# Kernel optimization log

Hardware: AMD Instinct MI355X
Metric: run time of the kernel (lower is better)

Reference implementation:

```python
import jax, jax.numpy as jnp
import numpy as np

EPS = 1e-20
K = 3        # kernel_size
STRIDE = 2
PAD = 1
DIL = 1
B, C, O, H, W = 4, 32, 32, 256, 256
HO = (H + 2 * PAD - DIL * (K - 1) - 1) // STRIDE + 1  # 128
WO = (W + 2 * PAD - DIL * (K - 1) - 1) // STRIDE + 1  # 128


def kernel_channels(x):
    """Unfold-like gather: [B,C,H,W] -> [B,C,K*K,HO,WO] (zero-padded)."""
    xp = jnp.pad(x, ((0, 0), (0, 0), (PAD, PAD), (PAD, PAD)))
    patches = [
        xp[:, :, i * DIL : i * DIL + (HO - 1) * STRIDE + 1 : STRIDE,
              j * DIL : j * DIL + (WO - 1) * STRIDE + 1 : STRIDE]
        for i in range(K) for j in range(K)
    ]
    return jnp.stack(patches, axis=2)


def setup_inputs() -> dict:
    key = jax.random.key(0)
    ks = jax.random.split(key, 11)
    return {
        "d":   jax.random.normal(ks[0], (B, C, H, W), jnp.float32),
        "cd":  jax.random.uniform(ks[1], (B, C, H, W), jnp.float32),
        "s":   jax.random.uniform(ks[2], (B, C, H, W), jnp.float32),
        "cs":  jax.random.uniform(ks[3], (B, C, H, W), jnp.float32),
        "gx":  jax.random.normal(ks[4], (B, C, H, W), jnp.float32),
        "cgx": jax.random.uniform(ks[5], (B, C, H, W), jnp.float32),
        "s_prod_roll": jax.random.uniform(ks[6], (B, C, K * K, HO, WO), jnp.float32),
        # learned parameters (raw; softplus applied in forward via EnforcePos)
        "w_prop":         jax.random.normal(ks[7], (1, C, 1, 1), jnp.float32) * 0.5,
        "spatial_weight": jax.random.normal(ks[8], (C, 1, K * K, 1, 1), jnp.float32) * 0.5,
        "channel_weight": jax.random.normal(ks[9], (O, C, 1, 1), jnp.float32) * 0.5,
        "bias":           jax.random.normal(ks[10], (1, O, 1, 1), jnp.float32) * 0.01,
    }


def reference(d, cd, s, cs, gx, cgx, s_prod_roll,
              w_prop, spatial_weight, channel_weight, bias):
    # EnforcePos: positive reparametrization of the weights
    wp = jax.nn.softplus(w_prop)                          # [1,C,1,1]
    sw = jax.nn.softplus(spatial_weight)[:, 0, :, 0, 0]   # [C,K*K]
    cw = jax.nn.softplus(channel_weight)[:, :, 0, 0]      # [O,C]

    # width-dim shift/pad (exactly matches F.pad(x[...,: -1], (0,1)) etc.)
    pad_r = lambda x: jnp.pad(x[:, :, :, :-1], ((0, 0), (0, 0), (0, 0), (0, 1)))
    pad_l = lambda x: jnp.pad(x[:, :, :, 1:],  ((0, 0), (0, 0), (0, 0), (1, 0)))
    d_left,  cd_left,  s_left  = pad_r(d), pad_r(cd), pad_r(s)
    d_right, cd_right, s_right = pad_l(d), pad_l(cd), pad_l(s)

    cgx_from_ds = s * s_left * s_right * cd_left * cd_right
    height = (cd_left * d_left + cd_right * d_right) / (cd_left + cd_right + EPS)
    gx_from_ds = (d_right - d_left) / 2 / (height + EPS)

    gx = (wp * cgx * gx + cgx_from_ds * gx_from_ds) / (wp * cgx + cgx_from_ds + EPS)
    cgx = (wp * cgx + cgx_from_ds) / (wp + 1.0)

    gx_roll = kernel_channels(gx)        # [B,C,K*K,HO,WO]
    cgx_roll = kernel_channels(cgx)
    cgx_prop = cgx_roll * s_prod_roll

    # spatial stage: grouped conv3d over kernel-channel dim == per-channel 9-tap reduce
    nom = jnp.einsum('bckhw,ck->bchw', cgx_prop * gx_roll, sw)
    den = jnp.einsum('bckhw,ck->bchw', cgx_prop, sw)
    gx_sp = nom / (den + EPS)
    cgx_sp = den / (jnp.sum(sw) + EPS)

    # channel stage: 1x1 conv2d (groups=1)
    nom2 = jnp.einsum('bchw,oc->bohw', cgx_sp * gx_sp, cw)
    den2 = jnp.einsum('bchw,oc->bohw', cgx_sp, cw)
    gx_out = nom2 / (den2 + EPS) + bias
    cgx_out = den2 / (jnp.sum(cw) + EPS)

    # devalue_pooled_confidence=True
    return gx_out * STRIDE, cgx_out / (STRIDE * STRIDE)
```

## Files before the change

### kernel.cpp

```cpp
#include <hip/hip_runtime.h>
#include <math.h>

#define EPSF 1e-20f
#define Bv 4
#define Cv 32
#define Ov 32
#define Hv 256
#define Wv 256
#define HOv 128
#define WOv 128
#define NPIX (HOv * WOv)
#define HALF_OUT (Bv * Ov * NPIX)

typedef float f4v __attribute__((ext_vector_type(4)));
typedef float f2v __attribute__((ext_vector_type(2)));

__device__ __forceinline__ float softplus_f(float x) {
    return fmaxf(x, 0.0f) + log1pf(__expf(-fabsf(x)));
}
__device__ __forceinline__ float frcp(float x) {
    return __builtin_amdgcn_rcpf(x);
}

__device__ __forceinline__ float4 gload4(const float* p) {
    float4 r;
    asm volatile("global_load_dwordx4 %0, %1, off" : "=v"(r) : "v"(p));
    return r;
}
__device__ __forceinline__ float2 gload2(const float* p) {
    float2 r;
    asm volatile("global_load_dwordx2 %0, %1, off" : "=v"(r) : "v"(p));
    return r;
}
__device__ __forceinline__ void vm_drain() {
    asm volatile("s_waitcnt vmcnt(0)" ::: "memory");
    __builtin_amdgcn_sched_barrier(0);
}

#define WS_BUF_OFF 2048
#define WS_NEEDED (WS_BUF_OFF * 4 + (size_t)Bv * Cv * NPIX * 8)

__global__ void prep_kernel(const float* __restrict__ wp_raw,
                            const float* __restrict__ sw_raw,
                            const float* __restrict__ cw_raw,
                            float* __restrict__ ws) {
    __shared__ float red_sw[256];
    __shared__ float red_cw[256];
    const int t = threadIdx.x;
    float acc_sw = 0.f, acc_cw = 0.f;
    if (t < 32) ws[t] = softplus_f(wp_raw[t]);
    for (int i = t; i < 288; i += 256) {
        float v = softplus_f(sw_raw[i]);
        ws[32 + i] = v;
        acc_sw += v;
    }
    for (int i = t; i < 1024; i += 256) {
        float v = softplus_f(cw_raw[i]);
        ws[320 + i] = v;
        acc_cw += v;
    }
    red_sw[t] = acc_sw;
    red_cw[t] = acc_cw;
    __syncthreads();
    for (int st = 128; st > 0; st >>= 1) {
        if (t < st) { red_sw[t] += red_sw[t + st]; red_cw[t] += red_cw[t + st]; }
        __syncthreads();
    }
    if (t == 0) {
        ws[1344] = 1.0f / (red_sw[0] + EPSF);
        ws[1345] = 1.0f / (red_cw[0] + EPSF);
    }
}

__global__ __launch_bounds__(256, 2)
void k1_spatial(const float* __restrict__ d,  const float* __restrict__ cd,
                const float* __restrict__ s,  const float* __restrict__ gx,
                const float* __restrict__ cgx, const float* __restrict__ sprod,
                const float* __restrict__ ws, float2* __restrict__ buf) {
    __shared__ float lds[16128];
    float* inL = lds;
    float* gaL = lds + 11520;
    float* caL = lds + 13824;

    const int t  = threadIdx.x;
    const int l  = t & 63;
    const int q  = t >> 6;
    const int z  = blockIdx.x >> 5;
    const int rt = blockIdx.x & 31;
    const int c  = z & 31;

    const float wpc = ws[c];
    const float inv_wp1 = frcp(wpc + 1.0f);
    const float inv_sumsw = ws[1344];
    const float* sw_c = ws + 32 + c * 9;

    const int ho0     = rt * 4;
    const int h_top   = 2 * ho0 - 1;
    const bool top    = (rt == 0);
    const int h_start = top ? 0 : h_top;
    const int nf4     = top ? 512 : 576;
    const int dof     = top ? 256 : 0;
    const int gbase   = z * (Hv * Wv) + h_start * Wv;

    float4 st[5][3];
#pragma unroll
    for (int a = 0; a < 5; ++a) {
        const float* gp = (a == 0) ? d : (a == 1) ? cd : (a == 2) ? s
                        : (a == 3) ? gx : cgx;
#pragma unroll
        for (int k = 0; k < 3; ++k) {
            const int o = t + k * 256;
            if (o < nf4) st[a][k] = gload4(gp + gbase + 4 * o);
        }
    }
    const int ho  = ho0 + q;
    const int sp0 = (z * 9 * HOv + ho) * WOv + 2 * l;
    f2v sp[9];
#pragma unroll
    for (int k = 0; k < 9; ++k)
        sp[k] = __builtin_nontemporal_load(
                    (const f2v*)(sprod + sp0 + k * NPIX));

    vm_drain();

#pragma unroll
    for (int a = 0; a < 5; ++a) {
#pragma unroll
        for (int k = 0; k < 3; ++k) {
            const int o = t + k * 256;
            if (o < nf4)
                *(float4*)(inL + a * 2304 + dof + 4 * o) = st[a][k];
        }
    }
    __syncthreads();

#pragma unroll
    for (int j = 0; j < 9; ++j) {
        const int o = j * 256 + t;
        const float dV  = inL[0 * 2304 + o];
        const float cdV = inL[1 * 2304 + o];
        const float sV  = inL[2 * 2304 + o];
        const float gV  = inL[3 * 2304 + o];
        const float cV  = inL[4 * 2304 + o];
        const bool mL = (t != Wv - 1);
        const bool mR = (t != 0);
        const float dL  = mL ? dV  : 0.f;
        const float cdL = mL ? cdV : 0.f;
        const float sL  = mL ? sV  : 0.f;
        const float dR  = mR ? dV  : 0.f;
        const float cdR = mR ? cdV : 0.f;
        const float sR  = mR ? sV  : 0.f;
        const float cgx_ds = sV * sL * sR * cdL * cdR;
        const float height = (cdL * dL + cdR * dR) * frcp(cdL + cdR + EPSF);
        const float gx_ds  = (dR - dL) * 0.5f * frcp(height + EPSF);
        const float a_ = wpc * cV;
        const float g_ = (a_ * gV + cgx_ds * gx_ds) * frcp(a_ + cgx_ds + EPSF);
        const float c_ = (a_ + cgx_ds) * inv_wp1;
        const bool vrow = (j > 0) || !top;
        gaL[o] = vrow ? g_ : 0.f;
        caL[o] = vrow ? c_ : 0.f;
    }
    __syncthreads();

    float n0 = 0.f, d0 = 0.f, n1 = 0.f, d1 = 0.f;
#pragma unroll
    for (int ki = 0; ki < 3; ++ki) {
        const int ro = (2 * q + ki) * 256;
        const float4 g4 = *(const float4*)(gaL + ro + 4 * l);
        const float4 c4 = *(const float4*)(caL + ro + 4 * l);
        const int eo = ro + (l ? 4 * l - 1 : 0);
        float geL = gaL[eo];
        float ceL = caL[eo];
        geL = l ? geL : 0.f;
        ceL = l ? ceL : 0.f;
        const float sw0 = sw_c[3 * ki + 0];
        const float sw1 = sw_c[3 * ki + 1];
        const float sw2 = sw_c[3 * ki + 2];
        float cp;
        cp = ceL  * sp[3 * ki + 0].x * sw0; d0 += cp; n0 = fmaf(cp, geL,  n0);
        cp = c4.x * sp[3 * ki + 1].x * sw1; d0 += cp; n0 = fmaf(cp, g4.x, n0);
        cp = c4.y * sp[3 * ki + 2].x * sw2; d0 += cp; n0 = fmaf(cp, g4.y, n0);
        cp = c4.y * sp[3 * ki + 0].y * sw0; d1 += cp; n1 = fmaf(cp, g4.y, n1);
        cp = c4.z * sp[3 * ki + 1].y * sw1; d1 += cp; n1 = fmaf(cp, g4.z, n1);
        cp = c4.w * sp[3 * ki + 2].y * sw2; d1 += cp; n1 = fmaf(cp, g4.w, n1);
    }
    const float gx0 = n0 * frcp(d0 + EPSF);
    const float cg0 = d0 * inv_sumsw;
    const float gx1 = n1 * frcp(d1 + EPSF);
    const float cg1 = d1 * inv_sumsw;
    float4 ov = {cg0 * gx0, cg0, cg1 * gx1, cg1};
    *(float4*)(buf + (size_t)z * NPIX + ho * WOv + 2 * l) = ov;
}

__global__ __launch_bounds__(256, 2)
void k2_channel(const float2* __restrict__ buf, const float* __restrict__ ws,
                const float* __restrict__ bias, float* __restrict__ out) {
    const int pg  = blockIdx.x * 256 + threadIdx.x;
    const int b   = pg >> 14;
    const int pp  = pg & (NPIX - 1);
    const int grp = blockIdx.y;
    const float* cw_t = ws + 320;
    const float inv_sumcw = ws[1345];

    const int cbase = b * Cv * NPIX + pp;

    float2 v[Cv];
#pragma unroll
    for (int cc = 0; cc < Cv; ++cc)
        v[cc] = gload2((const float*)(buf + cbase + cc * NPIX));

    vm_drain();

    float nom2[16], den2[16];
#pragma unroll
    for (int i = 0; i < 16; ++i) { nom2[i] = 0.f; den2[i] = 0.f; }

#pragma unroll
    for (int cc = 0; cc < Cv; ++cc) {
#pragma unroll
        for (int oi = 0; oi < 16; ++oi) {
            const float w_ = cw_t[(grp * 16 + oi) * Cv + cc];
            nom2[oi] = fmaf(v[cc].x, w_, nom2[oi]);
            den2[oi] = fmaf(v[cc].y, w_, den2[oi]);
        }
    }
#pragma unroll
    for (int oi = 0; oi < 16; ++oi) {
        const int o = grp * 16 + oi;
        const int p = (b * Ov + o) * NPIX + pp;
        const float dn = den2[oi];
        const float g  = nom2[oi] * frcp(dn + EPSF) + bias[o];
        __builtin_nontemporal_store(g * 2.0f, out + p);
        __builtin_nontemporal_store(dn * inv_sumcw * 0.25f, out + HALF_OUT + p);
    }
}

#define TH 4
#define TW 32
#define IH 9
#define IW 65
#define IWP 66
#define NTILE (IH * IW)

__global__ __launch_bounds__(128)
void main_kernel(const float* __restrict__ d,  const float* __restrict__ cd,
                 const float* __restrict__ s,  const float* __restrict__ gx,
                 const float* __restrict__ cgx, const float* __restrict__ sprod,
                 const float* __restrict__ bias, const float* __restrict__ ws,
                 float* __restrict__ out) {
    __shared__ float lgx[IH][IWP];
    __shared__ float lcgx[IH][IWP];
    const int t    = threadIdx.x;
    const int wo_l = t & 31;
    const int ho_l = t >> 5;
    const int wo0  = blockIdx.x * TW;
    const int ho0  = blockIdx.y * TH;
    const int b    = blockIdx.z;
    const int ho   = ho0 + ho_l;
    const int wo   = wo0 + wo_l;
    const float* sw_t = ws + 32;
    const float* cw_t = ws + 320;
    const float inv_sumsw = ws[1344];
    const float inv_sumcw = ws[1345];
    float nom2[Ov], den2[Ov];
#pragma unroll
    for (int o = 0; o < Ov; ++o) { nom2[o] = 0.f; den2[o] = 0.f; }
    const int h_base = 2 * ho0 - 1;
    const int w_base = 2 * wo0 - 1;
    for (int c = 0; c < Cv; ++c) {
        const float wpc = ws[c];
        const float inv_wp1 = frcp(wpc + 1.0f);
        const int ibase = (b * Cv + c) * (Hv * Wv);
        for (int idx = t; idx < NTILE; idx += 128) {
            const int r  = idx / IW;
            const int cc = idx - r * IW;
            const int h  = h_base + r;
            const int w  = w_base + cc;
            float gxn = 0.f, cgxn = 0.f;
            if ((unsigned)h < (unsigned)Hv && (unsigned)w < (unsigned)Wv) {
                const int p = ibase + h * Wv + w;
                const float dv = d[p], cdv = cd[p], sv = s[p];
                const float gxv = gx[p], cgxv = cgx[p];
                const bool mLb = (w != Wv - 1);
                const bool mRb = (w != 0);
                const float dL = mLb ? dv : 0.f, cdL = mLb ? cdv : 0.f, sL = mLb ? sv : 0.f;
                const float dR = mRb ? dv : 0.f, cdR = mRb ? cdv : 0.f, sR = mRb ? sv : 0.f;
                const float cgx_ds = sv * sL * sR * cdL * cdR;
                const float height = (cdL * dL + cdR * dR) * frcp(cdL + cdR + EPSF);
                const float gx_ds  = (dR - dL) * 0.5f * frcp(height + EPSF);
                const float a = wpc * cgxv;
                gxn  = (a * gxv + cgx_ds * gx_ds) * frcp(a + cgx_ds + EPSF);
                cgxn = (a + cgx_ds) * inv_wp1;
            }
            lgx[r][cc]  = gxn;
            lcgx[r][cc] = cgxn;
        }
        __syncthreads();
        const int spb = ((b * Cv + c) * 9 * HOv + ho) * WOv + wo;
        float nom = 0.f, den = 0.f;
#pragma unroll
        for (int k = 0; k < 9; ++k) {
            const int ki = k / 3;
            const int kj = k - ki * 3;
            const float gxr  = lgx[2 * ho_l + ki][2 * wo_l + kj];
            const float cgxr = lcgx[2 * ho_l + ki][2 * wo_l + kj];
            const float spv  = sprod[spb + k * NPIX];
            const float cp   = cgxr * spv * sw_t[c * 9 + k];
            den += cp;
            nom = fmaf(cp, gxr, nom);
        }
        const float gx_sp  = nom * frcp(den + EPSF);
        const float cgx_sp = den * inv_sumsw;
        const float t1 = cgx_sp * gx_sp;
#pragma unroll
        for (int o = 0; o < Ov; ++o) {
            const float w_ = cw_t[o * Cv + c];
            nom2[o] = fmaf(t1, w_, nom2[o]);
            den2[o] = fmaf(cgx_sp, w_, den2[o]);
        }
        __syncthreads();
    }
#pragma unroll
    for (int o = 0; o < Ov; ++o) {
        const int p = ((b * Ov + o) * HOv + ho) * WOv + wo;
        const float dn = den2[o];
        const float g  = nom2[o] * frcp(dn + EPSF) + bias[o];
        out[p]            = g * 2.0f;
        out[HALF_OUT + p] = dn * inv_sumcw * 0.25f;
    }
}

extern "C" void kernel_launch(void* const* d_in, const int* in_sizes, int n_in,
                              void* d_out, int out_size, void* d_ws, size_t ws_size,
                              hipStream_t stream) {
    const float* d_ptr    = (const float*)d_in[0];
    const float* cd_ptr   = (const float*)d_in[1];
    const float* s_ptr    = (const float*)d_in[2];
    const float* gx_ptr   = (const float*)d_in[4];
    const float* cgx_ptr  = (const float*)d_in[5];
    const float* sp_ptr   = (const float*)d_in[6];
    const float* wp_ptr   = (const float*)d_in[7];
    const float* sw_ptr   = (const float*)d_in[8];
    const float* cw_ptr   = (const float*)d_in[9];
    const float* bias_ptr = (const float*)d_in[10];
    float* out = (float*)d_out;
    float* ws  = (float*)d_ws;

    prep_kernel<<<1, 256, 0, stream>>>(wp_ptr, sw_ptr, cw_ptr, ws);

    if (ws_size >= WS_NEEDED) {
        float2* buf = (float2*)(ws + WS_BUF_OFF);
        k1_spatial<<<4096, 256, 0, stream>>>(d_ptr, cd_ptr, s_ptr, gx_ptr, cgx_ptr,
                                             sp_ptr, ws, buf);
        dim3 g2((Bv * NPIX) / 256, 2, 1);
        k2_channel<<<g2, 256, 0, stream>>>(buf, ws, bias_ptr, out);
    } else {
        dim3 grid(WOv / TW, HOv / TH, Bv);
        main_kernel<<<grid, 128, 0, stream>>>(d_ptr, cd_ptr, s_ptr, gx_ptr, cgx_ptr,
                                              sp_ptr, bias_ptr, ws, out);
    }
}
```

Baseline: 265.2 us.

## Halve spatial tile height to two output rows, one pixel per thread

```diff
diff --git a/kernel.cpp b/kernel.cpp
--- a/kernel.cpp
+++ b/kernel.cpp
@@ -72,76 +72,70 @@
     }
 }
 
-__global__ __launch_bounds__(256, 2)
+__global__ __launch_bounds__(256, 4)
 void k1_spatial(const float* __restrict__ d,  const float* __restrict__ cd,
                 const float* __restrict__ s,  const float* __restrict__ gx,
                 const float* __restrict__ cgx, const float* __restrict__ sprod,
                 const float* __restrict__ ws, float2* __restrict__ buf) {
-    __shared__ float lds[16128];
+    __shared__ float lds[8960];
     float* inL = lds;
-    float* gaL = lds + 11520;
-    float* caL = lds + 13824;
-
-    const int t  = threadIdx.x;
-    const int l  = t & 63;
-    const int q  = t >> 6;
-    const int z  = blockIdx.x >> 5;
-    const int rt = blockIdx.x & 31;
-    const int c  = z & 31;
+    float* gaL = lds + 6400;
+    float* caL = lds + 7680;
+
+    const int t   = threadIdx.x;
+    const int z   = blockIdx.x >> 6;
+    const int rtp = blockIdx.x & 63;
+    const int c   = z & 31;
 
     const float wpc = ws[c];
     const float inv_wp1 = frcp(wpc + 1.0f);
     const float inv_sumsw = ws[1344];
     const float* sw_c = ws + 32 + c * 9;
 
-    const int ho0     = rt * 4;
-    const int h_top   = 2 * ho0 - 1;
-    const bool top    = (rt == 0);
+    const int ho0     = rtp * 2;
+    const int h_top   = 4 * rtp - 1;
+    const bool top    = (rtp == 0);
     const int h_start = top ? 0 : h_top;
-    const int nf4     = top ? 512 : 576;
+    const int nf4     = top ? 256 : 320;
     const int dof     = top ? 256 : 0;
     const int gbase   = z * (Hv * Wv) + h_start * Wv;
 
-    float4 st[5][3];
+    const int o2  = t + 256;
+    const int o2c = (o2 < nf4) ? o2 : (nf4 - 1);
+    float4 st[5][2];
 #pragma unroll
     for (int a = 0; a < 5; ++a) {
         const float* gp = (a == 0) ? d : (a == 1) ? cd : (a == 2) ? s
                         : (a == 3) ? gx : cgx;
-#pragma unroll
-        for (int k = 0; k < 3; ++k) {
-            const int o = t + k * 256;
-            if (o < nf4) st[a][k] = gload4(gp + gbase + 4 * o);
-        }
-    }
-    const int ho  = ho0 + q;
-    const int sp0 = (z * 9 * HOv + ho) * WOv + 2 * l;
-    f2v sp[9];
+        st[a][0] = gload4(gp + gbase + 4 * t);
+        st[a][1] = gload4(gp + gbase + 4 * o2c);
+    }
+    const int ho = ho0 + (t >> 7);
+    const int wo = t & 127;
+    const int sp0 = (z * 9 * HOv + ho) * WOv + wo;
+    float sp[9];
 #pragma unroll
     for (int k = 0; k < 9; ++k)
-        sp[k] = __builtin_nontemporal_load(
-                    (const f2v*)(sprod + sp0 + k * NPIX));
+        sp[k] = __builtin_nontemporal_load(sprod + sp0 + k * NPIX);
 
     vm_drain();
 
 #pragma unroll
     for (int a = 0; a < 5; ++a) {
-#pragma unroll
-        for (int k = 0; k < 3; ++k) {
-            const int o = t + k * 256;
-            if (o < nf4)
-                *(float4*)(inL + a * 2304 + dof + 4 * o) = st[a][k];
-        }
+        *(float4*)(inL + a * 1280 + dof + 4 * t) = st[a][0];
+        if (o2 < nf4)
+            *(float4*)(inL + a * 1280 + dof + 4 * o2) = st[a][1];
     }
     __syncthreads();
 
 #pragma unroll
-    for (int j = 0; j < 9; ++j) {
+    for (int j = 0; j < 5; ++j) {
         const int o = j * 256 + t;
-        const float dV  = inL[0 * 2304 + o];
-        const float cdV = inL[1 * 2304 + o];
-        const float sV  = inL[2 * 2304 + o];
-        const float gV  = inL[3 * 2304 + o];
-        const float cV  = inL[4 * 2304 + o];
+        const float dV  = inL[0 * 1280 + o];
+        const float cdV = inL[1 * 1280 + o];
+        const float sV  = inL[2 * 1280 + o];
+        const float gV  = inL[3 * 1280 + o];
+        const float cV  = inL[4 * 1280 + o];
         const bool mL = (t != Wv - 1);
         const bool mR = (t != 0);
         const float dL  = mL ? dV  : 0.f;
@@ -162,34 +156,30 @@
     }
     __syncthreads();
 
-    float n0 = 0.f, d0 = 0.f, n1 = 0.f, d1 = 0.f;
+    const int qq = t >> 7;
+    float n0 = 0.f, d0 = 0.f;
 #pragma unroll
     for (int ki = 0; ki < 3; ++ki) {
-        const int ro = (2 * q + ki) * 256;
-        const float4 g4 = *(const float4*)(gaL + ro + 4 * l);
-        const float4 c4 = *(const float4*)(caL + ro + 4 * l);
-        const int eo = ro + (l ? 4 * l - 1 : 0);
-        float geL = gaL[eo];
-        float ceL = caL[eo];
-        geL = l ? geL : 0.f;
-        ceL = l ? ceL : 0.f;
+        const int ro = (2 * qq + ki) * 256;
+        const int bidx = ro + 2 * wo;
+        float gm = gaL[wo ? bidx - 1 : 0];
+        float cm = caL[wo ? bidx - 1 : 0];
+        gm = wo ? gm : 0.f;
+        cm = wo ? cm : 0.f;
+        const float g0 = gaL[bidx],     c0 = caL[bidx];
+        const float g1 = gaL[bidx + 1], c1 = caL[bidx + 1];
         const float sw0 = sw_c[3 * ki + 0];
         const float sw1 = sw_c[3 * ki + 1];
         const float sw2 = sw_c[3 * ki + 2];
         float cp;
-        cp = ceL  * sp[3 * ki + 0].x * sw0; d0 += cp; n0 = fmaf(cp, geL,  n0);
-        cp = c4.x * sp[3 * ki + 1].x * sw1; d0 += cp; n0 = fmaf(cp, g4.x, n0);
-        cp = c4.y * sp[3 * ki + 2].x * sw2; d0 += cp; n0 = fmaf(cp, g4.y, n0);
-        cp = c4.y * sp[3 * ki + 0].y * sw0; d1 += cp; n1 = fmaf(cp, g4.y, n1);
-        cp = c4.z * sp[3 * ki + 1].y * sw1; d1 += cp; n1 = fmaf(cp, g4.z, n1);
-        cp = c4.w * sp[3 * ki + 2].y * sw2; d1 += cp; n1 = fmaf(cp, g4.w, n1);
+        cp = cm * sp[3 * ki + 0] * sw0; d0 += cp; n0 = fmaf(cp, gm, n0);
+        cp = c0 * sp[3 * ki + 1] * sw1; d0 += cp; n0 = fmaf(cp, g0, n0);
+        cp = c1 * sp[3 * ki + 2] * sw2; d0 += cp; n0 = fmaf(cp, g1, n0);
     }
     const float gx0 = n0 * frcp(d0 + EPSF);
     const float cg0 = d0 * inv_sumsw;
-    const float gx1 = n1 * frcp(d1 + EPSF);
-    const float cg1 = d1 * inv_sumsw;
-    float4 ov = {cg0 * gx0, cg0, cg1 * gx1, cg1};
-    *(float4*)(buf + (size_t)z * NPIX + ho * WOv + 2 * l) = ov;
+    float2 ov = {cg0 * gx0, cg0};
+    buf[(size_t)z * NPIX + ho * WOv + wo] = ov;
 }
 
 __global__ __launch_bounds__(256, 2)
@@ -350,7 +340,7 @@
 
     if (ws_size >= WS_NEEDED) {
         float2* buf = (float2*)(ws + WS_BUF_OFF);
-        k1_spatial<<<4096, 256, 0, stream>>>(d_ptr, cd_ptr, s_ptr, gx_ptr, cgx_ptr,
+        k1_spatial<<<8192, 256, 0, stream>>>(d_ptr, cd_ptr, s_ptr, gx_ptr, cgx_ptr,
                                              sp_ptr, ws, buf);
         dim3 g2((Bv * NPIX) / 256, 2, 1);
         k2_channel<<<g2, 256, 0, stream>>>(buf, ws, bias_ptr, out);
```

Result: no change. 267.6 us (+0.9%).
